# Kernel optimization log

Measured on AMD Instinct MI355X. Metric: run time of the kernel, lower is better.

The kernel has to match this reference:

```python
import jax, jax.numpy as jnp
import numpy as np


def gcn_conv(x, W, b, src, dst, edge_weight):
    """GCNConv: out = A_hat @ (x @ W) + b, with A_hat given as an edge list.
    x: [N, F_in], W: [F_in, F_out], src/dst: [E] int, edge_weight: [E]."""
    N = x.shape[0]
    support = x @ W                                   # [N, F_out] dense GEMM
    msgs = support[src] * edge_weight[:, None]        # [E, F_out] gather + scale
    agg = jax.ops.segment_sum(msgs, dst, num_segments=N)  # [N, F_out] scatter-add
    return agg + b


def setup_inputs() -> dict:
    key = jax.random.key(0)
    ks = jax.random.split(key, 8)
    N, E, F_IN, H, D = 100000, 1600000, 256, 128, 64
    feature = jax.random.normal(ks[0], (N, F_IN), dtype=jnp.float32)
    src = jax.random.randint(ks[1], (E,), 0, N)
    dst = jax.random.randint(ks[2], (E,), 0, N)
    edge_weight = jax.random.uniform(ks[3], (E,), dtype=jnp.float32)
    W1 = jax.random.normal(ks[4], (F_IN, H), dtype=jnp.float32) / np.sqrt(F_IN).astype(np.float32)
    b1 = jnp.zeros((H,), jnp.float32)
    W2 = jax.random.normal(ks[5], (H, D), dtype=jnp.float32) / np.sqrt(H).astype(np.float32)
    b2 = jnp.zeros((D,), jnp.float32)
    return {"feature": feature, "src": src, "dst": dst, "edge_weight": edge_weight,
            "W1": W1, "b1": b1, "W2": W2, "b2": b2}


def reference(feature, src, dst, edge_weight, W1, b1, W2, b2):
    # layer 1: GCNConv -> relu (dropout is identity in eval mode)
    x1 = jax.nn.relu(gcn_conv(feature, W1, b1, src, dst, edge_weight))
    # layer 2: GCNConv -> log_softmax over feature dim
    x2 = gcn_conv(x1, W2, b2, src, dst, edge_weight)
    return (x1, jax.nn.log_softmax(x2, axis=1))
```

## Files before the change

kernel.cpp:

```cpp
#include <hip/hip_runtime.h>
#include <hip/hip_bf16.h>
#include <type_traits>


typedef unsigned short u16;

__device__ __forceinline__ u16 f2bf(float x) {
    union { float f; unsigned u; } v; v.f = x;
    const unsigned r = v.u + 0x7FFFu + ((v.u >> 16) & 1u);
    return (u16)(r >> 16);
}
__device__ __forceinline__ float bf2f(unsigned h) {
    union { unsigned u; float f; } v; v.u = h << 16;
    return v.f;
}
__device__ __forceinline__ float uaf(unsigned u) {
    union { unsigned u; float f; } v; v.u = u;
    return v.f;
}
__device__ __forceinline__ unsigned fau(float f) {
    union { float f; unsigned u; } v; v.f = f;
    return v.u;
}

using short8  = __attribute__((ext_vector_type(8))) short;
using float4v = __attribute__((ext_vector_type(4))) float;

#define EPT 8

template <typename AT, int BNt>
__device__ __forceinline__ void gemm_body(
    const int bix, const AT* __restrict__ A, const u16* __restrict__ BT,
    u16* __restrict__ C, const int M, const int K)
{
    constexpr int BMt = 128;
    constexpr int WAVES_N = BNt / 64;
    constexpr int WROWS = 4 / WAVES_N;
    constexpr int WMF = BMt / (16 * WROWS);
    constexpr int WNF = 4;

    __shared__ __align__(16) u16 As[BMt * 32];
    __shared__ __align__(16) u16 Bs[BNt * 32];

    const int tid  = threadIdx.x;
    const int lane = tid & 63;
    const int w    = tid >> 6;
    const int m0   = bix * BMt;

    const int wm = (w % WROWS) * (WMF * 16);
    const int wn = (w / WROWS) * 64;

    const int fm = lane & 15;
    const int kh = lane >> 4;

    float4v acc[WMF][WNF] = {};

    for (int k0 = 0; k0 < K; k0 += 32) {
        __syncthreads();
        if constexpr (std::is_same<AT, float>::value) {
#pragma unroll
            for (int i = 0; i < 4; ++i) {
                const int s   = i * 256 + tid;
                const int row = s >> 3;
                const int seg = s & 7;
                const int gr  = min(m0 + row, M - 1);
                const float4 v = *(const float4*)&A[(size_t)gr * K + k0 + seg * 4];
                ushort4 o;
                o.x = f2bf(v.x); o.y = f2bf(v.y); o.z = f2bf(v.z); o.w = f2bf(v.w);
                *(ushort4*)&As[row * 32 + seg * 4] = o;
            }
        } else {
#pragma unroll
            for (int i = 0; i < 2; ++i) {
                const int s   = i * 256 + tid;
                const int row = s >> 2;
                const int seg = s & 3;
                const int gr  = min(m0 + row, M - 1);
                *(uint4*)&As[row * 32 + seg * 8] =
                    *(const uint4*)&A[(size_t)gr * K + k0 + seg * 8];
            }
        }
#pragma unroll
        for (int i = 0; i < BNt * 4 / 256; ++i) {
            const int s   = i * 256 + tid;
            const int row = s >> 2;
            const int seg = s & 3;
            *(uint4*)&Bs[row * 32 + seg * 8] =
                *(const uint4*)&BT[(size_t)row * K + k0 + seg * 8];
        }
        __syncthreads();

        short8 af[WMF], bfr[WNF];
#pragma unroll
        for (int i = 0; i < WMF; ++i)
            af[i] = *(const short8*)&As[(wm + i * 16 + fm) * 32 + kh * 8];
#pragma unroll
        for (int j = 0; j < WNF; ++j)
            bfr[j] = *(const short8*)&Bs[(wn + j * 16 + fm) * 32 + kh * 8];
#pragma unroll
        for (int i = 0; i < WMF; ++i)
#pragma unroll
            for (int j = 0; j < WNF; ++j)
                acc[i][j] = __builtin_amdgcn_mfma_f32_16x16x32_bf16(
                    af[i], bfr[j], acc[i][j], 0, 0, 0);
    }

#pragma unroll
    for (int i = 0; i < WMF; ++i) {
#pragma unroll
        for (int j = 0; j < WNF; ++j) {
            const int col = wn + j * 16 + fm;
#pragma unroll
            for (int r = 0; r < 4; ++r) {
                const int row = m0 + wm + i * 16 + kh * 4 + r;
                if (row < M) C[(size_t)row * BNt + col] = f2bf(acc[i][j][r]);
            }
        }
    }
}

__global__ __launch_bounds__(256) void gemm2_k(
    const u16* __restrict__ A, const u16* __restrict__ BT,
    u16* __restrict__ C, int M, int K)
{
    gemm_body<u16, 64>(blockIdx.x, A, BT, C, M, K);
}

__global__ __launch_bounds__(256) void tc_k(
    const float* __restrict__ W1, u16* __restrict__ W1T, int K1, int N1,
    const float* __restrict__ W2, u16* __restrict__ W2T, int K2, int N2)
{
    const int t = blockIdx.x * blockDim.x + threadIdx.x;
    const int tot1 = K1 * N1;
    if (t < tot1) {
        const int k = t % K1, nn = t / K1;
        W1T[(size_t)nn * K1 + k] = f2bf(W1[(size_t)k * N1 + nn]);
    } else {
        const int t2 = t - tot1;
        if (t2 < K2 * N2) {
            const int k = t2 % K2, nn = t2 / K2;
            W2T[(size_t)nn * K2 + k] = f2bf(W2[(size_t)k * N2 + nn]);
        }
    }
}

__global__ __launch_bounds__(256) void mega0_k(
    const int* __restrict__ dst, int* __restrict__ counts, int E4, int E,
    const float* __restrict__ A, const u16* __restrict__ BT,
    u16* __restrict__ C, int M, int K, int GA)
{
    const int b = blockIdx.x;
    int gemm_id = -1, hist_id;
    if (b < 2 * GA) {
        if ((b & 1) == 0) gemm_id = b >> 1;
        else hist_id = b >> 1;
    } else {
        hist_id = b - GA;
    }
    if (gemm_id >= 0) {
        gemm_body<float, 128>(gemm_id, A, BT, C, M, K);
        return;
    }
    const int t = hist_id * 256 + threadIdx.x;
    if (t < E4) {
        const int4 d = *(const int4*)&dst[t * 4];
        atomicAdd(&counts[d.x], 1);
        atomicAdd(&counts[d.y], 1);
        atomicAdd(&counts[d.z], 1);
        atomicAdd(&counts[d.w], 1);
    } else if (t == E4) {
        for (int e = E4 * 4; e < E; ++e) atomicAdd(&counts[dst[e]], 1);
    }
}

__global__ __launch_bounds__(256) void mega1_k(
    const int* __restrict__ src, const int* __restrict__ dst,
    const float* __restrict__ ew, int* __restrict__ cursor,
    uint2* __restrict__ epack, int E,
    const float* __restrict__ A, const u16* __restrict__ BT,
    u16* __restrict__ C, int M, int K, int GA, int GB2)
{
    const int b = blockIdx.x;
    int gemm_id = -1, ro_id;
    if (b < 2 * GB2) {
        if ((b & 1) == 0) gemm_id = b >> 1;
        else ro_id = b >> 1;
    } else {
        ro_id = b - GB2;
    }
    if (gemm_id >= 0) {
        gemm_body<float, 128>(GA + gemm_id, A, BT, C, M, K);
        return;
    }
    const int base = (ro_id * 256 + threadIdx.x) * EPT;
    if (base >= E) return;
    if (base + EPT <= E) {
        const int4 d0 = *(const int4*)&dst[base];
        const int4 d1 = *(const int4*)&dst[base + 4];
        const int4 s0 = *(const int4*)&src[base];
        const int4 s1 = *(const int4*)&src[base + 4];
        const float4 w0 = *(const float4*)&ew[base];
        const float4 w1 = *(const float4*)&ew[base + 4];
        int p[EPT];
        p[0] = atomicAdd(&cursor[d0.x], 1);
        p[1] = atomicAdd(&cursor[d0.y], 1);
        p[2] = atomicAdd(&cursor[d0.z], 1);
        p[3] = atomicAdd(&cursor[d0.w], 1);
        p[4] = atomicAdd(&cursor[d1.x], 1);
        p[5] = atomicAdd(&cursor[d1.y], 1);
        p[6] = atomicAdd(&cursor[d1.z], 1);
        p[7] = atomicAdd(&cursor[d1.w], 1);
        epack[p[0]] = make_uint2((unsigned)s0.x, fau(w0.x));
        epack[p[1]] = make_uint2((unsigned)s0.y, fau(w0.y));
        epack[p[2]] = make_uint2((unsigned)s0.z, fau(w0.z));
        epack[p[3]] = make_uint2((unsigned)s0.w, fau(w0.w));
        epack[p[4]] = make_uint2((unsigned)s1.x, fau(w1.x));
        epack[p[5]] = make_uint2((unsigned)s1.y, fau(w1.y));
        epack[p[6]] = make_uint2((unsigned)s1.z, fau(w1.z));
        epack[p[7]] = make_uint2((unsigned)s1.w, fau(w1.w));
    } else {
        for (int e = base; e < E; ++e) {
            const int p = atomicAdd(&cursor[dst[e]], 1);
            epack[p] = make_uint2((unsigned)src[e], fau(ew[e]));
        }
    }
}


#define SCAN_B 256
#define SCAN_I 8
#define SCAN_TILE (SCAN_B * SCAN_I)

__global__ __launch_bounds__(SCAN_B) void scan_pass1(
    const int* __restrict__ in, int* __restrict__ out,
    int* __restrict__ blockSums, int n)
{
    __shared__ int waveSums[SCAN_B / 64];
    const int tid = threadIdx.x;
    const int lane = tid & 63;
    const int wid = tid >> 6;
    const int base = blockIdx.x * SCAN_TILE + tid * SCAN_I;

    int items[SCAN_I];
    int tsum = 0;
#pragma unroll
    for (int i = 0; i < SCAN_I; ++i) {
        const int idx = base + i;
        items[i] = (idx < n) ? in[idx] : 0;
        tsum += items[i];
    }
    int x = tsum;
#pragma unroll
    for (int o = 1; o < 64; o <<= 1) {
        const int y = __shfl_up(x, o, 64);
        if (lane >= o) x += y;
    }
    if (lane == 63) waveSums[wid] = x;
    __syncthreads();
    if (tid == 0) {
        int acc = 0;
#pragma unroll
        for (int w = 0; w < SCAN_B / 64; ++w) {
            const int t = waveSums[w]; waveSums[w] = acc; acc += t;
        }
        blockSums[blockIdx.x] = acc;
    }
    __syncthreads();
    int texcl = x - tsum + waveSums[wid];
#pragma unroll
    for (int i = 0; i < SCAN_I; ++i) {
        const int idx = base + i;
        if (idx < n) out[idx] = texcl;
        texcl += items[i];
    }
}

__global__ void scan_pass2(int* __restrict__ blockSums, int nb)
{
    const int lane = threadIdx.x;
    int run = 0;
    for (int base = 0; base < nb; base += 64) {
        const int idx = base + lane;
        const int v = (idx < nb) ? blockSums[idx] : 0;
        int x = v;
#pragma unroll
        for (int o = 1; o < 64; o <<= 1) {
            const int y = __shfl_up(x, o, 64);
            if (lane >= o) x += y;
        }
        if (idx < nb) blockSums[idx] = run + x - v;
        run += __shfl(x, 63, 64);
    }
}

__global__ __launch_bounds__(SCAN_B) void scan_pass3(
    int* __restrict__ offs, int* __restrict__ cursor,
    const int* __restrict__ blockSums, int n, int total)
{
    const int idx = blockIdx.x * blockDim.x + threadIdx.x;
    if (idx < n) {
        const int v = offs[idx] + blockSums[idx / SCAN_TILE];
        offs[idx] = v;
        cursor[idx] = v;
    }
    if (idx == n) offs[n] = total;
}


__global__ __launch_bounds__(256) void agg_f128b(
    const u16* __restrict__ sup, const int* __restrict__ offs,
    const uint2* __restrict__ epack, const float* __restrict__ bias,
    float* __restrict__ out, u16* __restrict__ out_bf, int N)
{
    const int node = (blockIdx.x * blockDim.x + threadIdx.x) >> 4;
    const int hl = threadIdx.x & 15;
    if (node >= N) return;

    const int beg = offs[node];
    const int end = offs[node + 1];

    float a[2][8] = {};
    int j = beg;
    for (; j + 7 < end; j += 8) {
        uint2 e[8];
#pragma unroll
        for (int i = 0; i < 8; ++i) e[i] = epack[j + i];
        uint4 v[8];
#pragma unroll
        for (int i = 0; i < 8; ++i)
            v[i] = *(const uint4*)&sup[(size_t)e[i].x * 128 + hl * 8];
#pragma unroll
        for (int i = 0; i < 8; ++i) {
            const float w = uaf(e[i].y);
            float* acc = a[i & 1];
            acc[0] = fmaf(bf2f(v[i].x & 0xffffu), w, acc[0]);
            acc[1] = fmaf(bf2f(v[i].x >> 16),     w, acc[1]);
            acc[2] = fmaf(bf2f(v[i].y & 0xffffu), w, acc[2]);
            acc[3] = fmaf(bf2f(v[i].y >> 16),     w, acc[3]);
            acc[4] = fmaf(bf2f(v[i].z & 0xffffu), w, acc[4]);
            acc[5] = fmaf(bf2f(v[i].z >> 16),     w, acc[5]);
            acc[6] = fmaf(bf2f(v[i].w & 0xffffu), w, acc[6]);
            acc[7] = fmaf(bf2f(v[i].w >> 16),     w, acc[7]);
        }
    }
    for (; j < end; ++j) {
        const uint2 e0 = epack[j];
        const float w = uaf(e0.y);
        const uint4 v0 = *(const uint4*)&sup[(size_t)e0.x * 128 + hl * 8];
        a[0][0] = fmaf(bf2f(v0.x & 0xffffu), w, a[0][0]);
        a[0][1] = fmaf(bf2f(v0.x >> 16),     w, a[0][1]);
        a[0][2] = fmaf(bf2f(v0.y & 0xffffu), w, a[0][2]);
        a[0][3] = fmaf(bf2f(v0.y >> 16),     w, a[0][3]);
        a[0][4] = fmaf(bf2f(v0.z & 0xffffu), w, a[0][4]);
        a[0][5] = fmaf(bf2f(v0.z >> 16),     w, a[0][5]);
        a[0][6] = fmaf(bf2f(v0.w & 0xffffu), w, a[0][6]);
        a[0][7] = fmaf(bf2f(v0.w >> 16),     w, a[0][7]);
    }
    const float4 b0 = *(const float4*)&bias[hl * 8];
    const float4 b1 = *(const float4*)&bias[hl * 8 + 4];
    float o[8];
    o[0] = fmaxf(a[0][0] + a[1][0] + b0.x, 0.f);
    o[1] = fmaxf(a[0][1] + a[1][1] + b0.y, 0.f);
    o[2] = fmaxf(a[0][2] + a[1][2] + b0.z, 0.f);
    o[3] = fmaxf(a[0][3] + a[1][3] + b0.w, 0.f);
    o[4] = fmaxf(a[0][4] + a[1][4] + b1.x, 0.f);
    o[5] = fmaxf(a[0][5] + a[1][5] + b1.y, 0.f);
    o[6] = fmaxf(a[0][6] + a[1][6] + b1.z, 0.f);
    o[7] = fmaxf(a[0][7] + a[1][7] + b1.w, 0.f);
    float* orow = &out[(size_t)node * 128 + hl * 8];
    *(float4*)&orow[0] = make_float4(o[0], o[1], o[2], o[3]);
    *(float4*)&orow[4] = make_float4(o[4], o[5], o[6], o[7]);
    uint4 pb;
    pb.x = (unsigned)f2bf(o[0]) | ((unsigned)f2bf(o[1]) << 16);
    pb.y = (unsigned)f2bf(o[2]) | ((unsigned)f2bf(o[3]) << 16);
    pb.z = (unsigned)f2bf(o[4]) | ((unsigned)f2bf(o[5]) << 16);
    pb.w = (unsigned)f2bf(o[6]) | ((unsigned)f2bf(o[7]) << 16);
    *(uint4*)&out_bf[(size_t)node * 128 + hl * 8] = pb;
}

__global__ __launch_bounds__(256) void agg_f64_lsm(
    const u16* __restrict__ sup, const int* __restrict__ offs,
    const uint2* __restrict__ epack, const float* __restrict__ bias,
    float* __restrict__ out, int N)
{
    const int node = (blockIdx.x * blockDim.x + threadIdx.x) >> 4;
    const int hl = threadIdx.x & 15;
    if (node >= N) return;

    const int beg = offs[node];
    const int end = offs[node + 1];

    float a[2][4] = {};
    int j = beg;
    for (; j + 7 < end; j += 8) {
        uint2 e[8];
#pragma unroll
        for (int i = 0; i < 8; ++i) e[i] = epack[j + i];
        uint2 v[8];
#pragma unroll
        for (int i = 0; i < 8; ++i)
            v[i] = *(const uint2*)&sup[(size_t)e[i].x * 64 + hl * 4];
#pragma unroll
        for (int i = 0; i < 8; ++i) {
            const float w = uaf(e[i].y);
            float* acc = a[i & 1];
            acc[0] = fmaf(bf2f(v[i].x & 0xffffu), w, acc[0]);
            acc[1] = fmaf(bf2f(v[i].x >> 16),     w, acc[1]);
            acc[2] = fmaf(bf2f(v[i].y & 0xffffu), w, acc[2]);
            acc[3] = fmaf(bf2f(v[i].y >> 16),     w, acc[3]);
        }
    }
    for (; j < end; ++j) {
        const uint2 e0 = epack[j];
        const float w = uaf(e0.y);
        const uint2 v0 = *(const uint2*)&sup[(size_t)e0.x * 64 + hl * 4];
        a[0][0] = fmaf(bf2f(v0.x & 0xffffu), w, a[0][0]);
        a[0][1] = fmaf(bf2f(v0.x >> 16),     w, a[0][1]);
        a[0][2] = fmaf(bf2f(v0.y & 0xffffu), w, a[0][2]);
        a[0][3] = fmaf(bf2f(v0.y >> 16),     w, a[0][3]);
    }

    const float4 b4 = *(const float4*)&bias[hl * 4];
    float z[4];
    z[0] = a[0][0] + a[1][0] + b4.x;
    z[1] = a[0][1] + a[1][1] + b4.y;
    z[2] = a[0][2] + a[1][2] + b4.z;
    z[3] = a[0][3] + a[1][3] + b4.w;

    float m = fmaxf(fmaxf(z[0], z[1]), fmaxf(z[2], z[3]));
#pragma unroll
    for (int o = 8; o > 0; o >>= 1) m = fmaxf(m, __shfl_xor(m, o, 64));
    float s = __expf(z[0] - m) + __expf(z[1] - m) + __expf(z[2] - m) + __expf(z[3] - m);
#pragma unroll
    for (int o = 8; o > 0; o >>= 1) s += __shfl_xor(s, o, 64);
    const float ls = __logf(s);
    *(float4*)&out[(size_t)node * 64 + hl * 4] =
        make_float4(z[0] - m - ls, z[1] - m - ls, z[2] - m - ls, z[3] - m - ls);
}


extern "C" void kernel_launch(void* const* d_in, const int* in_sizes, int n_in,
                              void* d_out, int out_size, void* d_ws, size_t ws_size,
                              hipStream_t stream) {
    const float* feature = (const float*)d_in[0];
    const int*   src     = (const int*)d_in[1];
    const int*   dst     = (const int*)d_in[2];
    const float* ew      = (const float*)d_in[3];
    const float* W1      = (const float*)d_in[4];
    const float* b1      = (const float*)d_in[5];
    const float* W2      = (const float*)d_in[6];
    const float* b2      = (const float*)d_in[7];

    const int E    = in_sizes[1];
    const int H    = in_sizes[5];
    const int D    = in_sizes[7];
    const int F_IN = in_sizes[4] / H;
    const int N    = in_sizes[0] / F_IN;

    float* out_x1 = (float*)d_out;
    float* out_x2 = (float*)d_out + (size_t)N * H;

    char* ws = (char*)d_ws;
    auto carve = [&](size_t bytes) {
        char* p = ws;
        ws += (bytes + 15) & ~(size_t)15;
        return p;
    };
    int*   counts    = (int*)  carve((size_t)N * sizeof(int));
    int*   offs      = (int*)  carve((size_t)(N + 1) * sizeof(int));
    int*   cursor    = (int*)  carve((size_t)N * sizeof(int));
    int*   blockSums = (int*)  carve(4096 * sizeof(int));
    uint2* epack     = (uint2*)carve((size_t)E * sizeof(uint2));
    u16*   W1T       = (u16*)  carve((size_t)H * F_IN * sizeof(u16));
    u16*   W2T       = (u16*)  carve((size_t)D * H * sizeof(u16));
    u16*   supbf     = (u16*)  carve((size_t)N * H * sizeof(u16));
    u16*   x1bf      = (u16*)  carve((size_t)N * H * sizeof(u16));

    const int GB  = (N + 127) / 128;
    const int GA  = GB / 2;
    const int GB2 = GB - GA;

    tc_k<<<(F_IN * H + H * D + 255) / 256, 256, 0, stream>>>(
        W1, W1T, F_IN, H, W2, W2T, H, D);

    hipMemsetAsync(counts, 0, (size_t)N * sizeof(int), stream);

    const int E4 = E / 4;
    const int HB = (E4 + 256) / 256;
    mega0_k<<<HB + GA, 256, 0, stream>>>(
        dst, counts, E4, E, feature, W1T, supbf, N, F_IN, GA);

    const int nScanBlocks = (N + SCAN_TILE - 1) / SCAN_TILE;
    scan_pass1<<<nScanBlocks, SCAN_B, 0, stream>>>(counts, offs, blockSums, N);
    scan_pass2<<<1, 64, 0, stream>>>(blockSums, nScanBlocks);
    scan_pass3<<<(N + 1 + SCAN_B - 1) / SCAN_B, SCAN_B, 0, stream>>>(
        offs, cursor, blockSums, N, E);

    {
        const int RB = ((E + EPT - 1) / EPT + 255) / 256;
        mega1_k<<<RB + GB2, 256, 0, stream>>>(
            src, dst, ew, cursor, epack, E,
            feature, W1T, supbf, N, F_IN, GA, GB2);
    }

    agg_f128b<<<(N * 16 + 255) / 256, 256, 0, stream>>>(
        supbf, offs, epack, b1, out_x1, x1bf, N);

    gemm2_k<<<(N + 127) / 128, 256, 0, stream>>>(x1bf, W2T, supbf, N, H);
    agg_f64_lsm<<<(N * 16 + 255) / 256, 256, 0, stream>>>(
        supbf, offs, epack, b2, out_x2, N);
}
```

Measured before the change: 491.8 us.

## Replace global-atomic CSR build with two-level LDS-histogram bucket sort

Replaces the global-atomic histogram plus global-atomic scatter of edges into CSR with a two-pass radix-style sort. Pass one buckets edges by dst>>8 using per-block shared-memory histograms, followed by a scan over the bucket-major count matrix. Pass two refines each bucket by the low byte of dst in shared memory, and this refinement runs interleaved with the layer-1 GEMM blocks in one launch. The aim is to cut contended global atomics and random scattered writes, at the cost of an extra pass over edge data and temporary buffers aliased onto x1bf. The weight transpose is also folded into the first sort kernel.

```diff
diff --git a/kernel.cpp b/kernel.cpp
--- a/kernel.cpp
+++ b/kernel.cpp
@@ -4,6 +4,7 @@
 
 
 typedef unsigned short u16;
+typedef unsigned char  u8;
 
 __device__ __forceinline__ u16 f2bf(float x) {
     union { float f; unsigned u; } v; v.f = x;
@@ -26,7 +27,7 @@
 using short8  = __attribute__((ext_vector_type(8))) short;
 using float4v = __attribute__((ext_vector_type(4))) float;
 
-#define EPT 8
+#define TILE_A 8192
 
 template <typename AT, int BNt>
 __device__ __forceinline__ void gemm_body(
@@ -126,104 +127,40 @@
     gemm_body<u16, 64>(blockIdx.x, A, BT, C, M, K);
 }
 
-__global__ __launch_bounds__(256) void tc_k(
+__global__ __launch_bounds__(256) void sortA1_k(
+    const int* __restrict__ dst, int* __restrict__ G, int E, int NBLK, int NB,
     const float* __restrict__ W1, u16* __restrict__ W1T, int K1, int N1,
     const float* __restrict__ W2, u16* __restrict__ W2T, int K2, int N2)
 {
-    const int t = blockIdx.x * blockDim.x + threadIdx.x;
-    const int tot1 = K1 * N1;
-    if (t < tot1) {
-        const int k = t % K1, nn = t / K1;
-        W1T[(size_t)nn * K1 + k] = f2bf(W1[(size_t)k * N1 + nn]);
-    } else {
-        const int t2 = t - tot1;
-        if (t2 < K2 * N2) {
-            const int k = t2 % K2, nn = t2 / K2;
-            W2T[(size_t)nn * K2 + k] = f2bf(W2[(size_t)k * N2 + nn]);
-        }
-    }
-}
-
-__global__ __launch_bounds__(256) void mega0_k(
-    const int* __restrict__ dst, int* __restrict__ counts, int E4, int E,
-    const float* __restrict__ A, const u16* __restrict__ BT,
-    u16* __restrict__ C, int M, int K, int GA)
-{
     const int b = blockIdx.x;
-    int gemm_id = -1, hist_id;
-    if (b < 2 * GA) {
-        if ((b & 1) == 0) gemm_id = b >> 1;
-        else hist_id = b >> 1;
-    } else {
-        hist_id = b - GA;
-    }
-    if (gemm_id >= 0) {
-        gemm_body<float, 128>(gemm_id, A, BT, C, M, K);
+    if (b >= NBLK) {
+        const int t = (b - NBLK) * 256 + threadIdx.x;
+        const int tot1 = K1 * N1;
+        if (t < tot1) {
+            const int k = t % K1, nn = t / K1;
+            W1T[(size_t)nn * K1 + k] = f2bf(W1[(size_t)k * N1 + nn]);
+        } else {
+            const int t2 = t - tot1;
+            if (t2 < K2 * N2) {
+                const int k = t2 % K2, nn = t2 / K2;
+                W2T[(size_t)nn * K2 + k] = f2bf(W2[(size_t)k * N2 + nn]);
+            }
+        }
         return;
     }
-    const int t = hist_id * 256 + threadIdx.x;
-    if (t < E4) {
-        const int4 d = *(const int4*)&dst[t * 4];
-        atomicAdd(&counts[d.x], 1);
-        atomicAdd(&counts[d.y], 1);
-        atomicAdd(&counts[d.z], 1);
-        atomicAdd(&counts[d.w], 1);
-    } else if (t == E4) {
-        for (int e = E4 * 4; e < E; ++e) atomicAdd(&counts[dst[e]], 1);
-    }
-}
-
-__global__ __launch_bounds__(256) void mega1_k(
-    const int* __restrict__ src, const int* __restrict__ dst,
-    const float* __restrict__ ew, int* __restrict__ cursor,
-    uint2* __restrict__ epack, int E,
-    const float* __restrict__ A, const u16* __restrict__ BT,
-    u16* __restrict__ C, int M, int K, int GA, int GB2)
-{
-    const int b = blockIdx.x;
-    int gemm_id = -1, ro_id;
-    if (b < 2 * GB2) {
-        if ((b & 1) == 0) gemm_id = b >> 1;
-        else ro_id = b >> 1;
-    } else {
-        ro_id = b - GB2;
-    }
-    if (gemm_id >= 0) {
-        gemm_body<float, 128>(GA + gemm_id, A, BT, C, M, K);
-        return;
-    }
-    const int base = (ro_id * 256 + threadIdx.x) * EPT;
-    if (base >= E) return;
-    if (base + EPT <= E) {
-        const int4 d0 = *(const int4*)&dst[base];
-        const int4 d1 = *(const int4*)&dst[base + 4];
-        const int4 s0 = *(const int4*)&src[base];
-        const int4 s1 = *(const int4*)&src[base + 4];
-        const float4 w0 = *(const float4*)&ew[base];
-        const float4 w1 = *(const float4*)&ew[base + 4];
-        int p[EPT];
-        p[0] = atomicAdd(&cursor[d0.x], 1);
-        p[1] = atomicAdd(&cursor[d0.y], 1);
-        p[2] = atomicAdd(&cursor[d0.z], 1);
-        p[3] = atomicAdd(&cursor[d0.w], 1);
-        p[4] = atomicAdd(&cursor[d1.x], 1);
-        p[5] = atomicAdd(&cursor[d1.y], 1);
-        p[6] = atomicAdd(&cursor[d1.z], 1);
-        p[7] = atomicAdd(&cursor[d1.w], 1);
-        epack[p[0]] = make_uint2((unsigned)s0.x, fau(w0.x));
-        epack[p[1]] = make_uint2((unsigned)s0.y, fau(w0.y));
-        epack[p[2]] = make_uint2((unsigned)s0.z, fau(w0.z));
-        epack[p[3]] = make_uint2((unsigned)s0.w, fau(w0.w));
-        epack[p[4]] = make_uint2((unsigned)s1.x, fau(w1.x));
-        epack[p[5]] = make_uint2((unsigned)s1.y, fau(w1.y));
-        epack[p[6]] = make_uint2((unsigned)s1.z, fau(w1.z));
-        epack[p[7]] = make_uint2((unsigned)s1.w, fau(w1.w));
-    } else {
-        for (int e = base; e < E; ++e) {
-            const int p = atomicAdd(&cursor[dst[e]], 1);
-            epack[p] = make_uint2((unsigned)src[e], fau(ew[e]));
-        }
-    }
+
+    __shared__ int hist[512];
+    for (int i = threadIdx.x; i < NB; i += 256) hist[i] = 0;
+    __syncthreads();
+    const int base = b * TILE_A;
+#pragma unroll 4
+    for (int i = 0; i < TILE_A; i += 256) {
+        const int e = base + i + threadIdx.x;
+        if (e < E) atomicAdd(&hist[((unsigned)dst[e]) >> 8], 1);
+    }
+    __syncthreads();
+    for (int i = threadIdx.x; i < NB; i += 256)
+        G[(size_t)i * NBLK + b] = hist[i];
 }
 
 
@@ -293,17 +230,100 @@
     }
 }
 
-__global__ __launch_bounds__(SCAN_B) void scan_pass3(
-    int* __restrict__ offs, int* __restrict__ cursor,
-    const int* __restrict__ blockSums, int n, int total)
+__global__ __launch_bounds__(SCAN_B) void scan3G_k(
+    int* __restrict__ G, const int* __restrict__ blockSums, int n,
+    int* __restrict__ offs, int N, int E)
 {
     const int idx = blockIdx.x * blockDim.x + threadIdx.x;
-    if (idx < n) {
-        const int v = offs[idx] + blockSums[idx / SCAN_TILE];
-        offs[idx] = v;
-        cursor[idx] = v;
-    }
-    if (idx == n) offs[n] = total;
+    if (idx < n) G[idx] += blockSums[idx / SCAN_TILE];
+    if (idx == 0) offs[N] = E;
+}
+
+__global__ __launch_bounds__(256) void sortA2_k(
+    const int* __restrict__ src, const int* __restrict__ dst,
+    const float* __restrict__ ew, const int* __restrict__ G,
+    uint2* __restrict__ eps, u8* __restrict__ ldst, int E, int NBLK, int NB)
+{
+    const int b = blockIdx.x;
+    __shared__ int cur[512];
+    for (int i = threadIdx.x; i < NB; i += 256)
+        cur[i] = G[(size_t)i * NBLK + b];
+    __syncthreads();
+    const int base = b * TILE_A;
+#pragma unroll 4
+    for (int i = 0; i < TILE_A; i += 256) {
+        const int e = base + i + threadIdx.x;
+        if (e < E) {
+            const int d = dst[e];
+            const int p = atomicAdd(&cur[((unsigned)d) >> 8], 1);
+            eps[p]  = make_uint2((unsigned)src[e], fau(ew[e]));
+            ldst[p] = (u8)(d & 255);
+        }
+    }
+}
+
+__global__ __launch_bounds__(256) void megaB_k(
+    const uint2* __restrict__ eps, const u8* __restrict__ ldst,
+    const int* __restrict__ G, int* __restrict__ offs,
+    uint2* __restrict__ epack, int E, int NBLK, int NB, int N,
+    const float* __restrict__ A, const u16* __restrict__ BT,
+    u16* __restrict__ C, int M, int K, int GB)
+{
+    const int b = blockIdx.x;
+    const int third = b / 3;
+    int sort_id = -1, gemm_id = -1;
+    if ((b % 3) == 0 && third < NB) sort_id = third;
+    else gemm_id = b - min((b + 2) / 3, NB);
+
+    if (gemm_id >= 0) {
+        if (gemm_id < GB) gemm_body<float, 128>(gemm_id, A, BT, C, M, K);
+        return;
+    }
+
+    const int tid = threadIdx.x;
+    const int sb = sort_id;
+    const int start = G[(size_t)sb * NBLK];
+    const int endv  = (sb + 1 < NB) ? G[(size_t)(sb + 1) * NBLK] : E;
+
+    __shared__ int h[256];
+    __shared__ int wsum[4];
+    h[tid] = 0;
+    __syncthreads();
+    for (int i = start + tid; i < endv; i += 256)
+        atomicAdd(&h[ldst[i]], 1);
+    __syncthreads();
+
+    const int lane = tid & 63;
+    const int w = tid >> 6;
+    const int v = h[tid];
+    int x = v;
+#pragma unroll
+    for (int o = 1; o < 64; o <<= 1) {
+        const int y = __shfl_up(x, o, 64);
+        if (lane >= o) x += y;
+    }
+    if (lane == 63) wsum[w] = x;
+    __syncthreads();
+    if (tid == 0) {
+        int a = 0;
+#pragma unroll
+        for (int q = 0; q < 4; ++q) { const int t = wsum[q]; wsum[q] = a; a += t; }
+    }
+    __syncthreads();
+    const int excl = start + (x - v) + wsum[w];
+
+    const int node = sb * 256 + tid;
+    if (node < N) offs[node] = excl;
+
+    __syncthreads();
+    h[tid] = excl;
+    __syncthreads();
+
+    for (int i = start + tid; i < endv; i += 256) {
+        const uint2 ep = eps[i];
+        const int p = atomicAdd(&h[ldst[i]], 1);
+        epack[p] = ep;
+    }
 }
 
 
@@ -460,47 +480,48 @@
     float* out_x1 = (float*)d_out;
     float* out_x2 = (float*)d_out + (size_t)N * H;
 
+    const int NB   = (N + 255) >> 8;
+    const int NBLK = (E + TILE_A - 1) / TILE_A;
+    const int nG   = NB * NBLK;
+    const int GB   = (N + 127) / 128;
+
     char* ws = (char*)d_ws;
     auto carve = [&](size_t bytes) {
         char* p = ws;
         ws += (bytes + 15) & ~(size_t)15;
         return p;
     };
-    int*   counts    = (int*)  carve((size_t)N * sizeof(int));
+    int*   G         = (int*)  carve((size_t)nG * sizeof(int));
+    int*   blockSums = (int*)  carve(4096 * sizeof(int));
     int*   offs      = (int*)  carve((size_t)(N + 1) * sizeof(int));
-    int*   cursor    = (int*)  carve((size_t)N * sizeof(int));
-    int*   blockSums = (int*)  carve(4096 * sizeof(int));
     uint2* epack     = (uint2*)carve((size_t)E * sizeof(uint2));
     u16*   W1T       = (u16*)  carve((size_t)H * F_IN * sizeof(u16));
     u16*   W2T       = (u16*)  carve((size_t)D * H * sizeof(u16));
     u16*   supbf     = (u16*)  carve((size_t)N * H * sizeof(u16));
     u16*   x1bf      = (u16*)  carve((size_t)N * H * sizeof(u16));
-
-    const int GB  = (N + 127) / 128;
-    const int GA  = GB / 2;
-    const int GB2 = GB - GA;
-
-    tc_k<<<(F_IN * H + H * D + 255) / 256, 256, 0, stream>>>(
-        W1, W1T, F_IN, H, W2, W2T, H, D);
-
-    hipMemsetAsync(counts, 0, (size_t)N * sizeof(int), stream);
-
-    const int E4 = E / 4;
-    const int HB = (E4 + 256) / 256;
-    mega0_k<<<HB + GA, 256, 0, stream>>>(
-        dst, counts, E4, E, feature, W1T, supbf, N, F_IN, GA);
-
-    const int nScanBlocks = (N + SCAN_TILE - 1) / SCAN_TILE;
-    scan_pass1<<<nScanBlocks, SCAN_B, 0, stream>>>(counts, offs, blockSums, N);
+    uint2* eps  = (uint2*)x1bf;
+    u8*    ldst = (u8*)x1bf + (size_t)E * sizeof(uint2);
+
+    {
+        const int TCB = (F_IN * H + H * D + 255) / 256;
+        sortA1_k<<<NBLK + TCB, 256, 0, stream>>>(
+            dst, G, E, NBLK, NB, W1, W1T, F_IN, H, W2, W2T, H, D);
+    }
+
+    const int nScanBlocks = (nG + SCAN_TILE - 1) / SCAN_TILE;
+    scan_pass1<<<nScanBlocks, SCAN_B, 0, stream>>>(G, G, blockSums, nG);
     scan_pass2<<<1, 64, 0, stream>>>(blockSums, nScanBlocks);
-    scan_pass3<<<(N + 1 + SCAN_B - 1) / SCAN_B, SCAN_B, 0, stream>>>(
-        offs, cursor, blockSums, N, E);
+    scan3G_k<<<(nG + SCAN_B - 1) / SCAN_B, SCAN_B, 0, stream>>>(
+        G, blockSums, nG, offs, N, E);
+
+    sortA2_k<<<NBLK, 256, 0, stream>>>(src, dst, ew, G, eps, ldst, E, NBLK, NB);
 
     {
-        const int RB = ((E + EPT - 1) / EPT + 255) / 256;
-        mega1_k<<<RB + GB2, 256, 0, stream>>>(
-            src, dst, ew, cursor, epack, E,
-            feature, W1T, supbf, N, F_IN, GA, GB2);
+        int grid = NB + GB;
+        if (grid < 3 * NB - 2) grid = 3 * NB - 2;
+        megaB_k<<<grid, 256, 0, stream>>>(
+            eps, ldst, G, offs, epack, E, NBLK, NB, N,
+            feature, W1T, supbf, N, F_IN, GB);
     }
 
     agg_f128b<<<(N * 16 + 255) / 256, 256, 0, stream>>>(
```

New measurement: 405.9 us. -17.5%, faster.
